# Kernel optimization log

Measured on AMD Instinct MI355X. Metric: run time of the kernel, lower is better.

Reference implementation:

```python
import jax, jax.numpy as jnp
import numpy as np

AUG = 8     # augmented_dim
NSUB = 4    # fixed Bosh3 substeps per save interval (replaces adaptive PID controller)


def setup_inputs() -> dict:
    key = jax.random.key(0)
    ks = jax.random.split(key, 8)
    B, T, DATA, WIDTH = 256, 64, 256, 256
    D = DATA + AUG
    ts = jnp.linspace(0.0, 1.0, T, dtype=jnp.float32)
    xs = jax.random.uniform(ks[0], (B, DATA), dtype=jnp.float32)
    a_sample = jax.random.normal(ks[1], (B,), dtype=jnp.float32)

    def lin(k, fan_in, fan_out):
        lim = 1.0 / np.sqrt(fan_in)
        kw, kb = jax.random.split(k)
        W = jax.random.uniform(kw, (fan_out, fan_in), minval=-lim, maxval=lim, dtype=jnp.float32)
        b = jax.random.uniform(kb, (fan_out,), minval=-lim, maxval=lim, dtype=jnp.float32)
        return W, b

    W0, b0 = lin(ks[2], D, WIDTH)
    W1, b1 = lin(ks[3], WIDTH, WIDTH)
    W2, b2 = lin(ks[4], WIDTH, WIDTH)
    W3, b3 = lin(ks[5], WIDTH, D)
    return dict(ts=ts, xs=xs, a_sample=a_sample,
                W0=W0, b0=b0, W1=W1, b1=b1, W2=W2, b2=b2, W3=W3, b3=b3)


def reference(ts, xs, a_sample, W0, b0, W1, b1, W2, b2, W3, b3):
    B = xs.shape[0]

    def f(y):  # autonomous vector field: MLP(y), batched over B
        h = jnp.tanh(y @ W0.T + b0)
        h = jnp.tanh(h @ W1.T + b1)
        h = jnp.tanh(h @ W2.T + b2)
        return h @ W3.T + b3

    # y0 = concat(a * exp(-0.1*t0) * sin(pi*xs), zeros(AUG))
    u0 = jnp.sin(jnp.pi * xs)
    scale = (a_sample * jnp.exp(-0.1 * ts[0]))[:, None]
    y0 = jnp.concatenate([scale * u0, jnp.zeros((B, AUG), xs.dtype)], axis=-1)  # [B, D]

    @jax.checkpoint
    def bosh3_step(y, h):
        k1 = f(y)
        k2 = f(y + 0.5 * h * k1)
        k3 = f(y + 0.75 * h * k2)
        return y + h * ((2.0 / 9.0) * k1 + (1.0 / 3.0) * k2 + (4.0 / 9.0) * k3)

    def interval(y, dt):
        h = dt / NSUB
        y = jax.lax.fori_loop(0, NSUB, lambda i, yy: bosh3_step(yy, h), y)
        return y, y

    dts = ts[1:] - ts[:-1]
    _, ys_tail = jax.lax.scan(interval, y0, dts)             # [T-1, B, D]
    ys = jnp.concatenate([y0[None], ys_tail], axis=0)        # [T, B, D]
    ys = jnp.transpose(ys, (1, 0, 2))[..., :-AUG]            # [B, T, data_size]
    return ys
```

## Files before the change

### kernel.cpp

```cpp
#include <hip/hip_runtime.h>
#include <cmath>

#define NB   256
#define NT   64
#define DATA 256
#define DD   264
#define NSUB 4
#define NTH  1024
#define NW   16
#define PI_F 3.14159265358979323846f

#define WS_W0B 0
#define WS_W1B (WS_W0B + 136 * 256)
#define WS_W2B (WS_W1B + 128 * 256)
#define WS_W3B (WS_W2B + 128 * 256)
#define WS_W3T (WS_W3B + 128 * 256)

#define L_W1B  0
#define L_PS   (L_W1B + 128 * 256)
#define L_Y    (L_PS + NW * 272)
#define L_IN   (L_Y + 272)
#define L_ACC  (L_IN + 272)
#define L_HA   (L_ACC + 272)
#define L_HB   (L_HA + 272)
#define L_B0   (L_HB + 272)
#define L_B1   (L_B0 + 256)
#define L_B2   (L_B1 + 256)
#define L_B3   (L_B2 + 256)
#define LDS_WORDS (L_B3 + 272)

#define UPK(u, f0, f1)                                                        \
  const float f0 = __uint_as_float((u) << 16);                                \
  const float f1 = __uint_as_float((u) & 0xffff0000u);

#define FMA8(acc, u, f0, f1)                                                  \
  {                                                                           \
    UPK(u.x, c0, c1) UPK(u.y, c2, c3) UPK(u.z, c4, c5) UPK(u.w, c6, c7)       \
    acc.x = fmaf(c0, f0, acc.x); acc.y = fmaf(c1, f0, acc.y);                 \
    acc.z = fmaf(c2, f0, acc.z); acc.w = fmaf(c3, f0, acc.w);                 \
    acc.x = fmaf(c4, f1, acc.x); acc.y = fmaf(c5, f1, acc.y);                 \
    acc.z = fmaf(c6, f1, acc.z); acc.w = fmaf(c7, f1, acc.w);                 \
  }

__device__ __forceinline__ unsigned bf16rn(float f) {
  unsigned u = __float_as_uint(f);
  return (u + 0x7fffu + ((u >> 16) & 1u)) >> 16;
}
__device__ __forceinline__ unsigned pk2(float lo, float hi) {
  return bf16rn(lo) | (bf16rn(hi) << 16);
}

__global__ void prep(const float* __restrict__ W0, const float* __restrict__ W1,
                     const float* __restrict__ W2, const float* __restrict__ W3,
                     unsigned* __restrict__ wsu) {
  int tid = blockIdx.x * blockDim.x + threadIdx.x;
  int stride = gridDim.x * blockDim.x;
  for (int i = tid; i < 136 * 256; i += stride) {
    int kk = i >> 8, r = i & 255, lq = r >> 2, j = r & 3;
    int k  = 2 * kk + (j >> 1);
    int c0 = 4 * lq + (j & 1) * 2;
    float lo = (k < DD) ? W0[c0 * DD + k] : 0.f;
    float hi = (k < DD) ? W0[(c0 + 1) * DD + k] : 0.f;
    wsu[WS_W0B + i] = pk2(lo, hi);
  }
  for (int i = tid; i < 128 * 256; i += stride) {
    int kk = i >> 8, r = i & 255, lq = r >> 2, j = r & 3;
    int k  = 2 * kk + (j >> 1);
    int c0 = 4 * lq + (j & 1) * 2;
    wsu[WS_W1B + i] = pk2(W1[c0 * 256 + k], W1[(c0 + 1) * 256 + k]);
    wsu[WS_W2B + i] = pk2(W2[c0 * 256 + k], W2[(c0 + 1) * 256 + k]);
    wsu[WS_W3B + i] = pk2(W3[c0 * 256 + k], W3[(c0 + 1) * 256 + k]);
  }
  for (int i = tid; i < 128 * 16; i += stride) {
    int kk = i >> 4, r = i & 15, lq = r >> 2, j = r & 3;
    int k  = 2 * kk + (j >> 1);
    int c0 = 256 + 4 * lq + (j & 1) * 2;
    float lo = (c0 < DD) ? W3[c0 * 256 + k] : 0.f;
    float hi = (c0 + 1 < DD) ? W3[(c0 + 1) * 256 + k] : 0.f;
    wsu[WS_W3T + i] = pk2(lo, hi);
  }
}

__global__ __launch_bounds__(NTH) void node_integrate(
    const float* __restrict__ ts, const float* __restrict__ xs,
    const float* __restrict__ a_sample,
    const float* __restrict__ b0g, const float* __restrict__ b1g,
    const float* __restrict__ b2g, const float* __restrict__ b3g,
    const unsigned* __restrict__ wsu, float* __restrict__ out) {
  extern __shared__ float sm[];
  unsigned* smu = (unsigned*)sm;
  const int b   = blockIdx.x;
  const int tid = threadIdx.x;
  const int w   = tid >> 6;
  const int l   = tid & 63;

  for (int i = tid; i < 256; i += NTH) {
    sm[L_B0 + i] = b0g[i];
    sm[L_B1 + i] = b1g[i];
    sm[L_B2 + i] = b2g[i];
  }
  for (int i = tid; i < 272; i += NTH) sm[L_B3 + i] = (i < DD) ? b3g[i] : 0.f;
  {
    const uint4* src = (const uint4*)(wsu + WS_W1B);
    uint4* dst = (uint4*)(smu + L_W1B);
    for (int i = tid; i < 128 * 64; i += NTH) dst[i] = src[i];
  }
  {
    const float sc = a_sample[b] * expf(-0.1f * ts[0]);
    for (int i = tid; i < 272; i += NTH) {
      float v = 0.f;
      if (i < DATA) v = sc * sinf(PI_F * xs[(size_t)b * DATA + i]);
      sm[L_Y + i]  = v;
      sm[L_IN + i] = 0.f;
    }
  }
  __syncthreads();

  if (tid < DATA) out[((size_t)b * NT) * DATA + tid] = sm[L_Y + tid];

  float4* ps4 = (float4*)(sm + L_PS);
  const uint4* w0b4 = (const uint4*)(wsu + WS_W0B);
  const uint4* w2b4 = (const uint4*)(wsu + WS_W2B);
  const uint4* w3b4 = (const uint4*)(wsu + WS_W3B);
  const uint4* w3t4 = (const uint4*)(wsu + WS_W3T);
  const uint4* w1l4 = (const uint4*)(smu + L_W1B);

#pragma unroll 1
  for (int t = 0; t < NT - 1; ++t) {
    const float dt = ts[t + 1] - ts[t];
    const float h  = dt * (1.0f / NSUB);
#pragma unroll 1
    for (int sub = 0; sub < NSUB; ++sub) {
#pragma unroll 1
      for (int st = 0; st < 3; ++st) {
        const float* finp = sm + ((st == 0) ? L_Y : L_IN);

        {
          float4 acc; acc.x = acc.y = acc.z = acc.w = 0.f;
#pragma unroll 4
          for (int i = 0; i < 8; ++i) {
            const int kk = w + 16 * i;
            const uint4 u = w0b4[kk * 64 + l];
            const float f0 = finp[2 * kk], f1 = finp[2 * kk + 1];
            FMA8(acc, u, f0, f1)
          }
          if (w < 8) {
            const int kk = 128 + w;
            const uint4 u = w0b4[kk * 64 + l];
            const float f0 = finp[2 * kk], f1 = finp[2 * kk + 1];
            FMA8(acc, u, f0, f1)
          }
          ps4[w * 68 + l] = acc;
        }
        __syncthreads();
        if (tid < 256) {
          float sv = sm[L_B0 + tid];
#pragma unroll
          for (int ww = 0; ww < NW; ++ww) sv += sm[L_PS + ww * 272 + tid];
          sm[L_HA + tid] = tanhf(sv);
        }
        __syncthreads();

        {
          float4 acc; acc.x = acc.y = acc.z = acc.w = 0.f;
#pragma unroll 4
          for (int i = 0; i < 8; ++i) {
            const int kk = w + 16 * i;
            const uint4 u = w1l4[kk * 64 + l];
            const float f0 = sm[L_HA + 2 * kk], f1 = sm[L_HA + 2 * kk + 1];
            FMA8(acc, u, f0, f1)
          }
          ps4[w * 68 + l] = acc;
        }
        __syncthreads();
        if (tid < 256) {
          float sv = sm[L_B1 + tid];
#pragma unroll
          for (int ww = 0; ww < NW; ++ww) sv += sm[L_PS + ww * 272 + tid];
          sm[L_HB + tid] = tanhf(sv);
        }
        __syncthreads();

        {
          float4 acc; acc.x = acc.y = acc.z = acc.w = 0.f;
#pragma unroll 4
          for (int i = 0; i < 8; ++i) {
            const int kk = w + 16 * i;
            const uint4 u = w2b4[kk * 64 + l];
            const float f0 = sm[L_HB + 2 * kk], f1 = sm[L_HB + 2 * kk + 1];
            FMA8(acc, u, f0, f1)
          }
          ps4[w * 68 + l] = acc;
        }
        __syncthreads();
        if (tid < 256) {
          float sv = sm[L_B2 + tid];
#pragma unroll
          for (int ww = 0; ww < NW; ++ww) sv += sm[L_PS + ww * 272 + tid];
          sm[L_HA + tid] = tanhf(sv);
        }
        __syncthreads();

        {
          float4 acc;  acc.x = acc.y = acc.z = acc.w = 0.f;
#pragma unroll 4
          for (int i = 0; i < 8; ++i) {
            const int kk = w + 16 * i;
            const uint4 u = w3b4[kk * 64 + l];
            const float f0 = sm[L_HA + 2 * kk], f1 = sm[L_HA + 2 * kk + 1];
            FMA8(acc, u, f0, f1)
          }
          ps4[w * 68 + l] = acc;
          if (l < 4) {
            float4 accx; accx.x = accx.y = accx.z = accx.w = 0.f;
#pragma unroll 4
            for (int i = 0; i < 8; ++i) {
              const int kk = w + 16 * i;
              const uint4 u = w3t4[kk * 4 + l];
              const float f0 = sm[L_HA + 2 * kk], f1 = sm[L_HA + 2 * kk + 1];
              FMA8(accx, u, f0, f1)
            }
            ps4[w * 68 + 64 + l] = accx;
          }
        }
        __syncthreads();
        if (tid < DD) {
          float kv = sm[L_B3 + tid];
#pragma unroll
          for (int ww = 0; ww < NW; ++ww) kv += sm[L_PS + ww * 272 + tid];
          if (st == 0) {
            sm[L_ACC + tid] = (2.0f / 9.0f) * kv;
            sm[L_IN + tid]  = sm[L_Y + tid] + 0.5f * h * kv;
          } else if (st == 1) {
            sm[L_ACC + tid] += (1.0f / 3.0f) * kv;
            sm[L_IN + tid]   = sm[L_Y + tid] + 0.75f * h * kv;
          } else {
            sm[L_Y + tid] += h * (sm[L_ACC + tid] + (4.0f / 9.0f) * kv);
          }
        }
        __syncthreads();
      }
    }
    if (tid < DATA) out[((size_t)b * NT + (t + 1)) * DATA + tid] = sm[L_Y + tid];
  }
}

extern "C" void kernel_launch(void* const* d_in, const int* in_sizes, int n_in,
                              void* d_out, int out_size, void* d_ws, size_t ws_size,
                              hipStream_t stream) {
  const float* ts = (const float*)d_in[0];
  const float* xs = (const float*)d_in[1];
  const float* a  = (const float*)d_in[2];
  const float* W0 = (const float*)d_in[3];
  const float* b0 = (const float*)d_in[4];
  const float* W1 = (const float*)d_in[5];
  const float* b1 = (const float*)d_in[6];
  const float* W2 = (const float*)d_in[7];
  const float* b2 = (const float*)d_in[8];
  const float* W3 = (const float*)d_in[9];
  const float* b3 = (const float*)d_in[10];
  unsigned* ws = (unsigned*)d_ws;
  float* out = (float*)d_out;

  const size_t lds_bytes = LDS_WORDS * sizeof(float);
  hipFuncSetAttribute(reinterpret_cast<const void*>(node_integrate),
                      hipFuncAttributeMaxDynamicSharedMemorySize,
                      (int)lds_bytes);

  hipLaunchKernelGGL(prep, dim3(256), dim3(256), 0, stream, W0, W1, W2, W3, ws);
  hipLaunchKernelGGL(node_integrate, dim3(NB), dim3(NTH), lds_bytes, stream,
                     ts, xs, a, b0, b1, b2, b3, ws, out);
}
```

Baseline: 5.491 ms.

## Switch MLP matvecs to fp16 packed dot2 with fp16-packed activations

Converts weights from bf16 to fp16, stored in plain row-pair layout, and replaces the per-element unpack-and-FMA with v_dot2 fp16 instructions that take packed weight and activation pairs. Activations and ODE stage inputs are packed to fp16 pairs in LDS via a lane shuffle after each tanh and stage update. This halves the LDS activation reads and cuts ALU work per weight, at the cost of fp16 range and rounding on activations and states, with the y state still kept in fp32.

```diff
diff --git a/kernel.cpp b/kernel.cpp
--- a/kernel.cpp
+++ b/kernel.cpp
@@ -10,45 +10,59 @@
 #define NW   16
 #define PI_F 3.14159265358979323846f
 
-#define WS_W0B 0
-#define WS_W1B (WS_W0B + 136 * 256)
-#define WS_W2B (WS_W1B + 128 * 256)
-#define WS_W3B (WS_W2B + 128 * 256)
-#define WS_W3T (WS_W3B + 128 * 256)
-
-#define L_W1B  0
-#define L_PS   (L_W1B + 128 * 256)
-#define L_Y    (L_PS + NW * 272)
-#define L_IN   (L_Y + 272)
-#define L_ACC  (L_IN + 272)
-#define L_HA   (L_ACC + 272)
-#define L_HB   (L_HA + 272)
-#define L_B0   (L_HB + 272)
+typedef _Float16 h2 __attribute__((ext_vector_type(2)));
+typedef __fp16   g2 __attribute__((ext_vector_type(2)));
+
+#define WS_W0  0
+#define WS_W1  (WS_W0 + 136 * 256)
+#define WS_W2  (WS_W1 + 128 * 256)
+#define WS_W3  (WS_W2 + 128 * 256)
+#define WS_W3T (WS_W3 + 128 * 256)
+
+#define L_W1   0
+#define L_PS   (L_W1 + 128 * 256)
+#define L_YP   (L_PS + NW * 272)
+#define L_INP  (L_YP + 136)
+#define L_HAP  (L_INP + 136)
+#define L_HBP  (L_HAP + 128)
+#define L_Y    (L_HBP + 128)
+#define L_ACC  (L_Y + 272)
+#define L_B0   (L_ACC + 272)
 #define L_B1   (L_B0 + 256)
 #define L_B2   (L_B1 + 256)
 #define L_B3   (L_B2 + 256)
 #define LDS_WORDS (L_B3 + 272)
 
-#define UPK(u, f0, f1)                                                        \
-  const float f0 = __uint_as_float((u) << 16);                                \
-  const float f1 = __uint_as_float((u) & 0xffff0000u);
-
-#define FMA8(acc, u, f0, f1)                                                  \
-  {                                                                           \
-    UPK(u.x, c0, c1) UPK(u.y, c2, c3) UPK(u.z, c4, c5) UPK(u.w, c6, c7)       \
-    acc.x = fmaf(c0, f0, acc.x); acc.y = fmaf(c1, f0, acc.y);                 \
-    acc.z = fmaf(c2, f0, acc.z); acc.w = fmaf(c3, f0, acc.w);                 \
-    acc.x = fmaf(c4, f1, acc.x); acc.y = fmaf(c5, f1, acc.y);                 \
-    acc.z = fmaf(c6, f1, acc.z); acc.w = fmaf(c7, f1, acc.w);                 \
-  }
-
-__device__ __forceinline__ unsigned bf16rn(float f) {
-  unsigned u = __float_as_uint(f);
-  return (u + 0x7fffu + ((u >> 16) & 1u)) >> 16;
-}
-__device__ __forceinline__ unsigned pk2(float lo, float hi) {
-  return bf16rn(lo) | (bf16rn(hi) << 16);
-}
+__device__ __forceinline__ float dot2(unsigned wu, unsigned hu, float c) {
+  h2 a = __builtin_bit_cast(h2, wu);
+  h2 b = __builtin_bit_cast(h2, hu);
+#if __has_builtin(__builtin_amdgcn_fdot2)
+  return __builtin_amdgcn_fdot2(a, b, c, false);
+#else
+  return c + (float)a[0] * (float)b[0] + (float)a[1] * (float)b[1];
+#endif
+}
+
+__device__ __forceinline__ unsigned pkh(float a, float b) {
+#if __has_builtin(__builtin_amdgcn_cvt_pkrtz)
+  g2 v = __builtin_amdgcn_cvt_pkrtz(a, b);
+  return __builtin_bit_cast(unsigned, v);
+#else
+  h2 v; v[0] = (_Float16)a; v[1] = (_Float16)b;
+  return __builtin_bit_cast(unsigned, v);
+#endif
+}
+
+__device__ __forceinline__ unsigned pkh_rne(float a, float b) {
+  h2 v; v[0] = (_Float16)a; v[1] = (_Float16)b;
+  return __builtin_bit_cast(unsigned, v);
+}
+
+#define DOT4(acc, u, hp)                                                      \
+  acc.x = dot2(u.x, hp, acc.x);                                               \
+  acc.y = dot2(u.y, hp, acc.y);                                               \
+  acc.z = dot2(u.z, hp, acc.z);                                               \
+  acc.w = dot2(u.w, hp, acc.w);
 
 __global__ void prep(const float* __restrict__ W0, const float* __restrict__ W1,
                      const float* __restrict__ W2, const float* __restrict__ W3,
@@ -56,28 +70,23 @@
   int tid = blockIdx.x * blockDim.x + threadIdx.x;
   int stride = gridDim.x * blockDim.x;
   for (int i = tid; i < 136 * 256; i += stride) {
-    int kk = i >> 8, r = i & 255, lq = r >> 2, j = r & 3;
-    int k  = 2 * kk + (j >> 1);
-    int c0 = 4 * lq + (j & 1) * 2;
-    float lo = (k < DD) ? W0[c0 * DD + k] : 0.f;
-    float hi = (k < DD) ? W0[(c0 + 1) * DD + k] : 0.f;
-    wsu[WS_W0B + i] = pk2(lo, hi);
+    int kk = i >> 8, j = i & 255;
+    int k0 = 2 * kk, k1 = 2 * kk + 1;
+    float lo = (k0 < DD) ? W0[j * DD + k0] : 0.f;
+    float hi = (k1 < DD) ? W0[j * DD + k1] : 0.f;
+    wsu[WS_W0 + i] = pkh_rne(lo, hi);
   }
   for (int i = tid; i < 128 * 256; i += stride) {
-    int kk = i >> 8, r = i & 255, lq = r >> 2, j = r & 3;
-    int k  = 2 * kk + (j >> 1);
-    int c0 = 4 * lq + (j & 1) * 2;
-    wsu[WS_W1B + i] = pk2(W1[c0 * 256 + k], W1[(c0 + 1) * 256 + k]);
-    wsu[WS_W2B + i] = pk2(W2[c0 * 256 + k], W2[(c0 + 1) * 256 + k]);
-    wsu[WS_W3B + i] = pk2(W3[c0 * 256 + k], W3[(c0 + 1) * 256 + k]);
+    int kk = i >> 8, j = i & 255;
+    wsu[WS_W1 + i] = pkh_rne(W1[j * 256 + 2 * kk], W1[j * 256 + 2 * kk + 1]);
+    wsu[WS_W2 + i] = pkh_rne(W2[j * 256 + 2 * kk], W2[j * 256 + 2 * kk + 1]);
+    wsu[WS_W3 + i] = pkh_rne(W3[j * 256 + 2 * kk], W3[j * 256 + 2 * kk + 1]);
   }
   for (int i = tid; i < 128 * 16; i += stride) {
-    int kk = i >> 4, r = i & 15, lq = r >> 2, j = r & 3;
-    int k  = 2 * kk + (j >> 1);
-    int c0 = 256 + 4 * lq + (j & 1) * 2;
-    float lo = (c0 < DD) ? W3[c0 * 256 + k] : 0.f;
-    float hi = (c0 + 1 < DD) ? W3[(c0 + 1) * 256 + k] : 0.f;
-    wsu[WS_W3T + i] = pk2(lo, hi);
+    int kk = i >> 4, c = 256 + (i & 15);
+    float lo = (c < DD) ? W3[c * 256 + 2 * kk] : 0.f;
+    float hi = (c < DD) ? W3[c * 256 + 2 * kk + 1] : 0.f;
+    wsu[WS_W3T + i] = pkh_rne(lo, hi);
   }
 }
 
@@ -101,8 +110,8 @@
   }
   for (int i = tid; i < 272; i += NTH) sm[L_B3 + i] = (i < DD) ? b3g[i] : 0.f;
   {
-    const uint4* src = (const uint4*)(wsu + WS_W1B);
-    uint4* dst = (uint4*)(smu + L_W1B);
+    const uint4* src = (const uint4*)(wsu + WS_W1);
+    uint4* dst = (uint4*)(smu + L_W1);
     for (int i = tid; i < 128 * 64; i += NTH) dst[i] = src[i];
   }
   {
@@ -110,20 +119,24 @@
     for (int i = tid; i < 272; i += NTH) {
       float v = 0.f;
       if (i < DATA) v = sc * sinf(PI_F * xs[(size_t)b * DATA + i]);
-      sm[L_Y + i]  = v;
-      sm[L_IN + i] = 0.f;
+      sm[L_Y + i] = v;
     }
   }
   __syncthreads();
+  if (tid < 136) {
+    smu[L_YP + tid]  = pkh(sm[L_Y + 2 * tid], sm[L_Y + 2 * tid + 1]);
+    smu[L_INP + tid] = 0u;
+  }
+  __syncthreads();
 
   if (tid < DATA) out[((size_t)b * NT) * DATA + tid] = sm[L_Y + tid];
 
   float4* ps4 = (float4*)(sm + L_PS);
-  const uint4* w0b4 = (const uint4*)(wsu + WS_W0B);
-  const uint4* w2b4 = (const uint4*)(wsu + WS_W2B);
-  const uint4* w3b4 = (const uint4*)(wsu + WS_W3B);
+  const uint4* w0b4 = (const uint4*)(wsu + WS_W0);
+  const uint4* w2b4 = (const uint4*)(wsu + WS_W2);
+  const uint4* w3b4 = (const uint4*)(wsu + WS_W3);
   const uint4* w3t4 = (const uint4*)(wsu + WS_W3T);
-  const uint4* w1l4 = (const uint4*)(smu + L_W1B);
+  const uint4* w1l4 = (const uint4*)(smu + L_W1);
 
 #pragma unroll 1
   for (int t = 0; t < NT - 1; ++t) {
@@ -133,7 +146,7 @@
     for (int sub = 0; sub < NSUB; ++sub) {
 #pragma unroll 1
       for (int st = 0; st < 3; ++st) {
-        const float* finp = sm + ((st == 0) ? L_Y : L_IN);
+        const unsigned* finp = smu + ((st == 0) ? L_YP : L_INP);
 
         {
           float4 acc; acc.x = acc.y = acc.z = acc.w = 0.f;
@@ -141,14 +154,14 @@
           for (int i = 0; i < 8; ++i) {
             const int kk = w + 16 * i;
             const uint4 u = w0b4[kk * 64 + l];
-            const float f0 = finp[2 * kk], f1 = finp[2 * kk + 1];
-            FMA8(acc, u, f0, f1)
+            const unsigned hp = finp[kk];
+            DOT4(acc, u, hp)
           }
           if (w < 8) {
             const int kk = 128 + w;
             const uint4 u = w0b4[kk * 64 + l];
-            const float f0 = finp[2 * kk], f1 = finp[2 * kk + 1];
-            FMA8(acc, u, f0, f1)
+            const unsigned hp = finp[kk];
+            DOT4(acc, u, hp)
           }
           ps4[w * 68 + l] = acc;
         }
@@ -157,7 +170,9 @@
           float sv = sm[L_B0 + tid];
 #pragma unroll
           for (int ww = 0; ww < NW; ++ww) sv += sm[L_PS + ww * 272 + tid];
-          sm[L_HA + tid] = tanhf(sv);
+          const float hv = tanhf(sv);
+          const float ho = __shfl_xor(hv, 1);
+          if (!(tid & 1)) smu[L_HAP + (tid >> 1)] = pkh(hv, ho);
         }
         __syncthreads();
 
@@ -167,8 +182,8 @@
           for (int i = 0; i < 8; ++i) {
             const int kk = w + 16 * i;
             const uint4 u = w1l4[kk * 64 + l];
-            const float f0 = sm[L_HA + 2 * kk], f1 = sm[L_HA + 2 * kk + 1];
-            FMA8(acc, u, f0, f1)
+            const unsigned hp = smu[L_HAP + kk];
+            DOT4(acc, u, hp)
           }
           ps4[w * 68 + l] = acc;
         }
@@ -177,7 +192,9 @@
           float sv = sm[L_B1 + tid];
 #pragma unroll
           for (int ww = 0; ww < NW; ++ww) sv += sm[L_PS + ww * 272 + tid];
-          sm[L_HB + tid] = tanhf(sv);
+          const float hv = tanhf(sv);
+          const float ho = __shfl_xor(hv, 1);
+          if (!(tid & 1)) smu[L_HBP + (tid >> 1)] = pkh(hv, ho);
         }
         __syncthreads();
 
@@ -187,8 +204,8 @@
           for (int i = 0; i < 8; ++i) {
             const int kk = w + 16 * i;
             const uint4 u = w2b4[kk * 64 + l];
-            const float f0 = sm[L_HB + 2 * kk], f1 = sm[L_HB + 2 * kk + 1];
-            FMA8(acc, u, f0, f1)
+            const unsigned hp = smu[L_HBP + kk];
+            DOT4(acc, u, hp)
           }
           ps4[w * 68 + l] = acc;
         }
@@ -197,18 +214,20 @@
           float sv = sm[L_B2 + tid];
 #pragma unroll
           for (int ww = 0; ww < NW; ++ww) sv += sm[L_PS + ww * 272 + tid];
-          sm[L_HA + tid] = tanhf(sv);
-        }
-        __syncthreads();
-
-        {
-          float4 acc;  acc.x = acc.y = acc.z = acc.w = 0.f;
+          const float hv = tanhf(sv);
+          const float ho = __shfl_xor(hv, 1);
+          if (!(tid & 1)) smu[L_HAP + (tid >> 1)] = pkh(hv, ho);
+        }
+        __syncthreads();
+
+        {
+          float4 acc; acc.x = acc.y = acc.z = acc.w = 0.f;
 #pragma unroll 4
           for (int i = 0; i < 8; ++i) {
             const int kk = w + 16 * i;
             const uint4 u = w3b4[kk * 64 + l];
-            const float f0 = sm[L_HA + 2 * kk], f1 = sm[L_HA + 2 * kk + 1];
-            FMA8(acc, u, f0, f1)
+            const unsigned hp = smu[L_HAP + kk];
+            DOT4(acc, u, hp)
           }
           ps4[w * 68 + l] = acc;
           if (l < 4) {
@@ -217,8 +236,8 @@
             for (int i = 0; i < 8; ++i) {
               const int kk = w + 16 * i;
               const uint4 u = w3t4[kk * 4 + l];
-              const float f0 = sm[L_HA + 2 * kk], f1 = sm[L_HA + 2 * kk + 1];
-              FMA8(accx, u, f0, f1)
+              const unsigned hp = smu[L_HAP + kk];
+              DOT4(accx, u, hp)
             }
             ps4[w * 68 + 64 + l] = accx;
           }
@@ -228,14 +247,21 @@
           float kv = sm[L_B3 + tid];
 #pragma unroll
           for (int ww = 0; ww < NW; ++ww) kv += sm[L_PS + ww * 272 + tid];
+          float val;
           if (st == 0) {
             sm[L_ACC + tid] = (2.0f / 9.0f) * kv;
-            sm[L_IN + tid]  = sm[L_Y + tid] + 0.5f * h * kv;
+            val = sm[L_Y + tid] + 0.5f * h * kv;
           } else if (st == 1) {
             sm[L_ACC + tid] += (1.0f / 3.0f) * kv;
-            sm[L_IN + tid]   = sm[L_Y + tid] + 0.75f * h * kv;
+            val = sm[L_Y + tid] + 0.75f * h * kv;
           } else {
-            sm[L_Y + tid] += h * (sm[L_ACC + tid] + (4.0f / 9.0f) * kv);
+            val = sm[L_Y + tid] + h * (sm[L_ACC + tid] + (4.0f / 9.0f) * kv);
+            sm[L_Y + tid] = val;
+          }
+          const float vo = __shfl_xor(val, 1);
+          if (!(tid & 1)) {
+            const int dst = (st == 2) ? L_YP : L_INP;
+            smu[dst + (tid >> 1)] = pkh(val, vo);
           }
         }
         __syncthreads();
@@ -263,9 +289,9 @@
   float* out = (float*)d_out;
 
   const size_t lds_bytes = LDS_WORDS * sizeof(float);
-  hipFuncSetAttribute(reinterpret_cast<const void*>(node_integrate),
-                      hipFuncAttributeMaxDynamicSharedMemorySize,
-                      (int)lds_bytes);
+  (void)hipFuncSetAttribute(reinterpret_cast<const void*>(node_integrate),
+                            hipFuncAttributeMaxDynamicSharedMemorySize,
+                            (int)lds_bytes);
 
   hipLaunchKernelGGL(prep, dim3(256), dim3(256), 0, stream, W0, W1, W2, W3, ws);
   hipLaunchKernelGGL(node_integrate, dim3(NB), dim3(NTH), lds_bytes, stream,
```

Result: faster. 4.697 ms, median of 2 (-14.5%).
